# Kernel optimization log

Hardware: AMD Instinct MI355X
Metric: run time of the kernel (lower is better)

The kernel has to match this reference:

```python
import jax, jax.numpy as jnp
import numpy as np

D, H, E, K, N, PROJ = 512, 1024, 8, 2, 65536, 256
C = N * K // E  # expert capacity (capacity_factor=1.0 over the full token count)
LOG100 = float(np.log(100.0))


def _l2norm(v, axis=-1):
    return v / (jnp.linalg.norm(v, axis=axis, keepdims=True) + 1e-12)


def _moe(x, mask, Wp, bp, sim, temp, W1, b1, W2, b2):
    # tutel 'cosine_top' gate: cosine sim between projected tokens and expert embeddings,
    # scaled by clamped learned temperature.
    logits = _l2norm(x @ Wp + bp) @ _l2norm(sim, axis=0)
    logits = logits * jnp.exp(jnp.minimum(temp, LOG100))
    gates_all = jax.nn.softmax(logits, axis=-1)
    g, idx = jax.lax.top_k(gates_all, K)                      # [N,K]
    g = g / (jnp.sum(g, axis=-1, keepdims=True) + 1e-9)       # normalize top-k gates
    g = g * mask[:, None]                                     # zero out tokens not in this domain
    e = idx.reshape(-1)                                       # [N*K] expert id per slot
    gflat = g.reshape(-1)
    valid = jnp.repeat(mask, K)                               # [N*K]
    oh = jax.nn.one_hot(e, E, dtype=jnp.float32) * valid[:, None]
    pos = (jnp.cumsum(oh, axis=0) * oh).sum(-1).astype(jnp.int32) - 1  # slot within expert
    keep = ((pos >= 0) & (pos < C)).astype(x.dtype)           # drop overflow / masked tokens
    posc = jnp.clip(pos, 0, C - 1)
    tok = jnp.arange(N * K, dtype=jnp.int32) // K
    # dispatch -> [E,C,D]
    xd = jnp.zeros((E, C, D), x.dtype).at[e, posc].add(x[tok] * keep[:, None])
    # grouped expert FFN
    h = jax.nn.relu(jnp.einsum('ecd,edh->ech', xd, W1) + b1[:, None, :])
    y = jnp.einsum('ech,ehd->ecd', h, W2) + b2[:, None, :]
    # combine back to tokens
    out = jnp.zeros((N, D), x.dtype).at[tok].add(y[e, posc] * (gflat * keep)[:, None])
    return out


def _make_params(key):
    ks = jax.random.split(key, 4)
    Wp = jax.random.normal(ks[0], (D, PROJ), jnp.float32) * 0.02
    bp = jnp.zeros((PROJ,), jnp.float32)
    sim = jax.random.normal(ks[1], (PROJ, E), jnp.float32) * 0.02
    temp = jnp.asarray(np.log(10.0), jnp.float32)
    W1 = jax.random.normal(ks[2], (E, D, H), jnp.float32) * (1.0 / np.sqrt(D))
    b1 = jnp.zeros((E, H), jnp.float32)
    W2 = jax.random.normal(ks[3], (E, H, D), jnp.float32) * (1.0 / np.sqrt(H))
    b2 = jnp.zeros((E, D), jnp.float32)
    return Wp, bp, sim, temp, W1, b1, W2, b2


def setup_inputs():
    key = jax.random.key(0)
    kx, kl, k1, k2, k3, ksc = jax.random.split(key, 6)
    inp = {
        'x': jax.random.normal(kx, (N, D), jnp.float32),
        'domain_label': jax.random.randint(kl, (N,), 0, 2),
        'domain_scale': jax.random.normal(ksc, (1,), jnp.float32) * 0.1,
    }
    for name, k in (('sh', k1), ('day', k2), ('nt', k3)):
        Wp, bp, sim, temp, W1, b1, W2, b2 = _make_params(k)
        inp.update({name + '_Wp': Wp, name + '_bp': bp, name + '_sim': sim, name + '_temp': temp,
                    name + '_W1': W1, name + '_b1': b1, name + '_W2': W2, name + '_b2': b2})
    return inp


def reference(x, domain_label, domain_scale,
              sh_Wp, sh_bp, sh_sim, sh_temp, sh_W1, sh_b1, sh_W2, sh_b2,
              day_Wp, day_bp, day_sim, day_temp, day_W1, day_b1, day_W2, day_b2,
              nt_Wp, nt_bp, nt_sim, nt_temp, nt_W1, nt_b1, nt_W2, nt_b2):
    ones = jnp.ones((N,), jnp.float32)
    day = (domain_label == 0).astype(jnp.float32)
    night = (domain_label == 1).astype(jnp.float32)
    f_shared = _moe(x, ones, sh_Wp, sh_bp, sh_sim, sh_temp, sh_W1, sh_b1, sh_W2, sh_b2)
    f_domain = (_moe(x, day, day_Wp, day_bp, day_sim, day_temp, day_W1, day_b1, day_W2, day_b2)
                + _moe(x, night, nt_Wp, nt_bp, nt_sim, nt_temp, nt_W1, nt_b1, nt_W2, nt_b2))
    return f_shared + domain_scale * f_domain
```

## Files before the change

### kernel.cpp

```cpp
#include <hip/hip_runtime.h>

#define NTOK 65536
#define DDIM 512
#define HDIM 1024
#define NEXP 8
#define PROJ 256
#define CAP  16384
#define NSLOT (2*NTOK)
#define LOG100 4.605170185988091f

typedef __attribute__((ext_vector_type(8))) short bf16x8;
typedef __attribute__((ext_vector_type(4))) short short4v;
typedef __attribute__((ext_vector_type(4))) float f32x4;

__device__ inline float bf2f(unsigned short u){
    union { float f; unsigned int i; } c; c.i = ((unsigned int)u) << 16; return c.f;
}
__device__ inline unsigned short f2bf(float f){
    union { float f; unsigned int i; } c; c.f = f;
    unsigned int x = c.i;
    return (unsigned short)((x + 0x7fffu + ((x >> 16) & 1u)) >> 16);
}
__device__ inline void gload16(const void* g, void* lds){
    __builtin_amdgcn_global_load_lds(
        (const __attribute__((address_space(1))) unsigned int*)g,
        (__attribute__((address_space(3))) unsigned int*)lds, 16, 0, 0);
}

__global__ void init_k(const float4* __restrict__ x, ushort4* __restrict__ xb,
                       float4* __restrict__ out){
    long i = (long)blockIdx.x * 256 + threadIdx.x;
    float4 f = x[i];
    ushort4 u; u.x = f2bf(f.x); u.y = f2bf(f.y); u.z = f2bf(f.z); u.w = f2bf(f.w);
    xb[i] = u;
    out[i] = float4{0.f, 0.f, 0.f, 0.f};
}

__device__ inline void trans_body(const float* in, unsigned short* out, int R, int C){
    int rbase = blockIdx.y * 32, cbase = blockIdx.x * 32;
    if (rbase >= R || cbase >= C) return;
    __shared__ float tile[32][33];
    int tx = threadIdx.x, ty = threadIdx.y;
    #pragma unroll
    for (int i = 0; i < 4; i++)
        tile[ty + i*8][tx] = in[(long)(rbase + ty + i*8) * C + cbase + tx];
    __syncthreads();
    #pragma unroll
    for (int i = 0; i < 4; i++)
        out[(long)(cbase + ty + i*8) * R + rbase + tx] = f2bf(tile[tx][ty + i*8]);
}

__global__ __launch_bounds__(256)
void trans2_k(const float* __restrict__ W1, const float* __restrict__ W2,
              unsigned short* __restrict__ W1T, unsigned short* __restrict__ W2T)
{
    int z = blockIdx.z;
    if (z < 8) trans_body(W1 + (size_t)z*DDIM*HDIM, W1T + (size_t)z*DDIM*HDIM, DDIM, HDIM);
    else       trans_body(W2 + (size_t)(z-8)*DDIM*HDIM, W2T + (size_t)(z-8)*DDIM*HDIM, HDIM, DDIM);
}

struct W12P { const float* W1[3]; const float* W2[3]; };
__global__ __launch_bounds__(256)
void transW12all_k(W12P wp, unsigned short* __restrict__ W1T3, unsigned short* __restrict__ W2T3)
{
    int z = blockIdx.z, m = z >> 4, piece = z & 15;
    if (piece < 8)
        trans_body(wp.W1[m] + (size_t)piece*DDIM*HDIM,
                   W1T3 + ((size_t)m*8 + piece)*DDIM*HDIM, DDIM, HDIM);
    else
        trans_body(wp.W2[m] + (size_t)(piece-8)*DDIM*HDIM,
                   W2T3 + ((size_t)m*8 + piece-8)*DDIM*HDIM, HDIM, DDIM);
}

struct TpArgs { const float* Wp[3]; };
__global__ __launch_bounds__(256)
void transWp_k(TpArgs ta, unsigned short* __restrict__ WpT3)
{
    int m = blockIdx.z;
    trans_body(ta.Wp[m], WpT3 + (size_t)m*PROJ*DDIM, DDIM, PROJ);
}

struct SimArgs { const float* sim[3]; };
__global__ void simn3_k(SimArgs sa, float* __restrict__ simn3){
    __shared__ float red[256];
    const float* sim = sa.sim[blockIdx.x];
    float* simn = simn3 + (size_t)blockIdx.x * PROJ * NEXP;
    int j = threadIdx.x;
    for (int e = 0; e < NEXP; e++){
        float v = sim[j*NEXP + e];
        red[j] = v*v;
        __syncthreads();
        for (int s = 128; s > 0; s >>= 1){
            if (j < s) red[j] += red[j + s];
            __syncthreads();
        }
        float nrm = sqrtf(red[0]) + 1e-12f;
        __syncthreads();
        simn[j*NEXP + e] = v / nrm;
    }
}

struct WprodArgs { const float* Wp[3]; const float* bp[3]; };
__global__ __launch_bounds__(256)
void wprod_k(WprodArgs wa, const float* __restrict__ simn3,
             float* __restrict__ Wn3, float* __restrict__ bd3)
{
    int m = blockIdx.x;
    __shared__ float Sn[PROJ*NEXP];
    const float* Wp = wa.Wp[m];
    int t = threadIdx.x;
    for (int i = t; i < PROJ*NEXP; i += 256) Sn[i] = simn3[(size_t)m*PROJ*NEXP + i];
    __syncthreads();
    for (int r = t; r < DDIM; r += 256){
        float d[8];
        #pragma unroll
        for (int e = 0; e < 8; e++) d[e] = 0.f;
        for (int p = 0; p < PROJ; p++){
            float w = Wp[(size_t)r*PROJ + p];
            #pragma unroll
            for (int e = 0; e < 8; e++) d[e] = fmaf(w, Sn[p*8+e], d[e]);
        }
        #pragma unroll
        for (int e = 0; e < 8; e++) Wn3[((size_t)m*DDIM + r)*8 + e] = d[e];
    }
    if (t < 8){
        float s = 0.f;
        for (int p = 0; p < PROJ; p++) s = fmaf(wa.bp[m][p], Sn[p*8+t], s);
        bd3[m*8 + t] = s;
    }
}

struct PssArgs { const float* bp[3]; };
__global__ __launch_bounds__(256)
void pss_k(const unsigned short* __restrict__ WpT3, const unsigned short* __restrict__ xb,
           PssArgs pa, float* __restrict__ ssbuf)
{
    __shared__ __align__(16) short As[128*32];
    __shared__ __align__(16) short Bs[128*32];
    __shared__ float ssl[2][128];
    const int m = blockIdx.z;
    const int row0 = blockIdx.x * 128;
    const int n0 = blockIdx.y * 128;
    const unsigned short* AT = WpT3 + (size_t)m * PROJ * DDIM;
    const float* bp = pa.bp[m];

    const int t = threadIdx.x, w = t >> 6, l = t & 63;
    const int qrow = l >> 2, kc = (l & 3) * 8;
    long arowg[2], browg[2];
    #pragma unroll
    for (int q = 0; q < 2; q++){
        arowg[q] = (long)(row0 + w*32 + q*16 + qrow) * DDIM;
        browg[q] = (long)(n0   + w*32 + q*16 + qrow) * DDIM;
    }
    const int wm = (w >> 1) * 64, wn = (w & 1) * 64;
    const int fr = l & 15, fk = l >> 4;
    const int koff = fk * 8, fk4 = fk * 4;

    f32x4 acc[4][4];
    #pragma unroll
    for (int i = 0; i < 4; i++)
        #pragma unroll
        for (int j = 0; j < 4; j++) acc[i][j] = (f32x4){0.f, 0.f, 0.f, 0.f};

    for (int k0 = 0; k0 < DDIM; k0 += 32){
        __syncthreads();
        #pragma unroll
        for (int q = 0; q < 2; q++) gload16(AT + arowg[q] + k0 + kc, As + w*1024 + q*512);
        #pragma unroll
        for (int q = 0; q < 2; q++) gload16(xb + browg[q] + k0 + kc, Bs + w*1024 + q*512);
        __syncthreads();
        bf16x8 af[4], bfv[4];
        #pragma unroll
        for (int i = 0; i < 4; i++) af[i]  = *(const bf16x8*)&As[(wm + i*16 + fr)*32 + koff];
        #pragma unroll
        for (int j = 0; j < 4; j++) bfv[j] = *(const bf16x8*)&Bs[(wn + j*16 + fr)*32 + koff];
        #pragma unroll
        for (int i = 0; i < 4; i++)
            #pragma unroll
            for (int j = 0; j < 4; j++)
                acc[i][j] = __builtin_amdgcn_mfma_f32_16x16x32_bf16(af[i], bfv[j], acc[i][j], 0, 0, 0);
    }

    float part[4];
    #pragma unroll
    for (int j = 0; j < 4; j++){
        float s = 0.f;
        #pragma unroll
        for (int i = 0; i < 4; i++){
            int mc = row0 + wm + i*16 + fk4;
            float4 bb = *(const float4*)(bp + mc);
            float v0 = acc[i][j][0] + bb.x;
            float v1 = acc[i][j][1] + bb.y;
            float v2 = acc[i][j][2] + bb.z;
            float v3 = acc[i][j][3] + bb.w;
            s += v0*v0 + v1*v1 + v2*v2 + v3*v3;
        }
        s += __shfl_xor(s, 16, 64);
        s += __shfl_xor(s, 32, 64);
        part[j] = s;
    }
    if (fk == 0){
        #pragma unroll
        for (int j = 0; j < 4; j++) ssl[w >> 1][wn + j*16 + fr] = part[j];
    }
    __syncthreads();
    if (t < 128)
        ssbuf[((size_t)blockIdx.x*3 + m)*NTOK + n0 + t] = ssl[0][t] + ssl[1][t];
}

struct GfArgs { const float* tp[3]; };
__global__ __launch_bounds__(256)
void gatefin2_k(const float* __restrict__ x, const int* __restrict__ label,
                const float* __restrict__ Wn3, const float* __restrict__ bd3,
                const float* __restrict__ ssbuf, GfArgs gf,
                int* __restrict__ idx3, float* __restrict__ gw3)
{
    __shared__ __align__(16) float Wl[3*512*12];
    const int t = threadIdx.x;
    for (int i = t; i < 3072; i += 256){
        float4 v = ((const float4*)Wn3)[i];
        int row = i >> 1, half = i & 1;
        *(float4*)&Wl[row*12 + half*4] = v;
    }
    __syncthreads();

    const int r = t & 7, q = t >> 3;
    const int n0 = blockIdx.x * 128;
    const int nb = n0 + q*4;

    float dots[4][3][8];
    #pragma unroll
    for (int a = 0; a < 4; a++)
        #pragma unroll
        for (int m = 0; m < 3; m++)
            #pragma unroll
            for (int e = 0; e < 8; e++) dots[a][m][e] = 0.f;

    #pragma unroll 4
    for (int i = 0; i < 16; i++){
        float4 xv[4];
        #pragma unroll
        for (int a = 0; a < 4; a++)
            xv[a] = ((const float4*)(x + (size_t)(nb + a)*DDIM))[r + 8*i];
        #pragma unroll
        for (int j = 0; j < 4; j++){
            int k = (r + 8*i)*4 + j;
            #pragma unroll
            for (int m = 0; m < 3; m++){
                const float* wr = &Wl[(m*512 + k)*12];
                float4 w0 = *(const float4*)wr;
                float4 w1 = *(const float4*)(wr + 4);
                #pragma unroll
                for (int a = 0; a < 4; a++){
                    float av = (j==0) ? xv[a].x : (j==1) ? xv[a].y : (j==2) ? xv[a].z : xv[a].w;
                    dots[a][m][0] = fmaf(av, w0.x, dots[a][m][0]);
                    dots[a][m][1] = fmaf(av, w0.y, dots[a][m][1]);
                    dots[a][m][2] = fmaf(av, w0.z, dots[a][m][2]);
                    dots[a][m][3] = fmaf(av, w0.w, dots[a][m][3]);
                    dots[a][m][4] = fmaf(av, w1.x, dots[a][m][4]);
                    dots[a][m][5] = fmaf(av, w1.y, dots[a][m][5]);
                    dots[a][m][6] = fmaf(av, w1.z, dots[a][m][6]);
                    dots[a][m][7] = fmaf(av, w1.w, dots[a][m][7]);
                }
            }
        }
    }
    #pragma unroll
    for (int o = 1; o <= 4; o <<= 1)
        #pragma unroll
        for (int a = 0; a < 4; a++)
            #pragma unroll
            for (int m = 0; m < 3; m++)
                #pragma unroll
                for (int e = 0; e < 8; e++)
                    dots[a][m][e] += __shfl_xor(dots[a][m][e], o, 64);

    if (r == 0){
        #pragma unroll
        for (int a = 0; a < 4; a++){
            int n = nb + a;
            int lab = label[n];
            #pragma unroll
            for (int m = 0; m < 3; m++){
                float ss = ssbuf[(0*3+m)*(size_t)NTOK + n] + ssbuf[(1*3+m)*(size_t)NTOK + n];
                float scale = expf(fminf(gf.tp[m][0], LOG100));
                float inv = scale / (sqrtf(ss) + 1e-12f);
                float l8[8], mx = -1e30f;
                #pragma unroll
                for (int e = 0; e < 8; e++){
                    l8[e] = (dots[a][m][e] + bd3[m*8+e]) * inv;
                    mx = fmaxf(mx, l8[e]);
                }
                float g[8], s = 0.f;
                #pragma unroll
                for (int e = 0; e < 8; e++){ g[e] = expf(l8[e] - mx); s += g[e]; }
                #pragma unroll
                for (int e = 0; e < 8; e++) g[e] /= s;
                int e0 = 0; float b0 = g[0];
                #pragma unroll
                for (int e = 1; e < 8; e++) if (g[e] > b0){ b0 = g[e]; e0 = e; }
                int e1 = (e0 == 0) ? 1 : 0; float b1v = g[e1];
                #pragma unroll
                for (int e = 0; e < 8; e++) if (e != e0 && g[e] > b1v){ b1v = g[e]; e1 = e; }
                float maskv = (m == 0) ? 1.f : ((lab == m - 1) ? 1.f : 0.f);
                float s2 = b0 + b1v + 1e-9f;
                size_t base = (size_t)m * NSLOT + 2*(size_t)n;
                gw3[base]   = b0 / s2 * maskv;
                gw3[base+1] = b1v / s2 * maskv;
                idx3[base]   = e0;
                idx3[base+1] = e1;
            }
        }
    }
}

template<int BGATHER, int OMODE>
__device__ __forceinline__
void gemm_core_t(short* As, short* Bs,
                 const unsigned short* __restrict__ AT, const unsigned short* __restrict__ Bv,
                 const float* __restrict__ bias, void* __restrict__ Cout,
                 int Kd, int Mld, int row0, int col0, int limitN,
                 const int* __restrict__ rowidx, const int* __restrict__ otok,
                 const float* __restrict__ gs)
{
    const int t = threadIdx.x;
    const int w = t >> 6, l = t & 63;
    const int qrow = l >> 2;
    const int kc = (l & 3) * 8;

    long arowg[2], browg[2];
    #pragma unroll
    for (int q = 0; q < 2; q++){
        arowg[q] = (long)(row0 + w*32 + q*16 + qrow) * Kd;
        int s = col0 + w*32 + q*16 + qrow;
        int gi = s;
        if (BGATHER) gi = (s < limitN) ? rowidx[s] : 0;
        browg[q] = (long)gi * Kd;
    }

    const int wm = (w >> 1) * 64, wn = (w & 1) * 64;
    const int fr = l & 15, fk = l >> 4;
    const int koff = fk * 8, fk4 = fk * 4;

    f32x4 acc[4][4];
    #pragma unroll
    for (int i = 0; i < 4; i++)
        #pragma unroll
        for (int j = 0; j < 4; j++) acc[i][j] = (f32x4){0.f, 0.f, 0.f, 0.f};

    for (int k0 = 0; k0 < Kd; k0 += 32){
        __syncthreads();
        #pragma unroll
        for (int q = 0; q < 2; q++) gload16(AT + arowg[q] + k0 + kc, As + w*1024 + q*512);
        #pragma unroll
        for (int q = 0; q < 2; q++) gload16(Bv + browg[q] + k0 + kc, Bs + w*1024 + q*512);
        __syncthreads();
        bf16x8 af[4], bfv[4];
        #pragma unroll
        for (int i = 0; i < 4; i++) af[i]  = *(const bf16x8*)&As[(wm + i*16 + fr)*32 + koff];
        #pragma unroll
        for (int j = 0; j < 4; j++) bfv[j] = *(const bf16x8*)&Bs[(wn + j*16 + fr)*32 + koff];
        #pragma unroll
        for (int i = 0; i < 4; i++)
            #pragma unroll
            for (int j = 0; j < 4; j++)
                acc[i][j] = __builtin_amdgcn_mfma_f32_16x16x32_bf16(af[i], bfv[j], acc[i][j], 0, 0, 0);
    }

    #pragma unroll
    for (int i = 0; i < 4; i++){
        const int mc = row0 + wm + i*16 + fk4;
        float4 bb = *(const float4*)(bias + mc);
        #pragma unroll
        for (int j = 0; j < 4; j++){
            int s = col0 + wn + j*16 + fr;
            if (s < limitN){
                if (OMODE == 1){
                    ushort4 u;
                    u.x = f2bf(fmaxf(acc[i][j][0] + bb.x, 0.f));
                    u.y = f2bf(fmaxf(acc[i][j][1] + bb.y, 0.f));
                    u.z = f2bf(fmaxf(acc[i][j][2] + bb.z, 0.f));
                    u.w = f2bf(fmaxf(acc[i][j][3] + bb.w, 0.f));
                    *(ushort4*)((unsigned short*)Cout + (long)s * Mld + mc) = u;
                } else {
                    int tk = otok[s];
                    float g = gs[s];
                    float* op = (float*)Cout + (long)tk * Mld + mc;
                    float4 c = *(const float4*)op;
                    c.x += g * (acc[i][j][0] + bb.x);
                    c.y += g * (acc[i][j][1] + bb.y);
                    c.z += g * (acc[i][j][2] + bb.z);
                    c.w += g * (acc[i][j][3] + bb.w);
                    *(float4*)op = c;
                }
            }
        }
    }
}

template<int BGATHER, int OMODE>
__device__ __forceinline__
void gemm_core_t64(short* As, short* Bs,
                   const unsigned short* __restrict__ AT, const unsigned short* __restrict__ Bv,
                   const float* __restrict__ bias, void* __restrict__ Cout,
                   int Kd, int Mld, int row0, int col0, int limitN,
                   const int* __restrict__ rowidx, const int* __restrict__ otok,
                   const float* __restrict__ gs)
{
    const int t = threadIdx.x;
    const int w = t >> 6, l = t & 63;
    const int qrow = l >> 2;
    const int seg = (l & 3) * 8;

    long arowg[2], browg[2];
    #pragma unroll
    for (int q = 0; q < 2; q++){
        arowg[q] = (long)(row0 + w*32 + q*16 + qrow) * Kd;
        int s = col0 + w*32 + q*16 + qrow;
        int gi = s;
        if (BGATHER) gi = (s < limitN) ? rowidx[s] : 0;
        browg[q] = (long)gi * Kd;
    }

    const int wm = (w >> 1) * 64, wn = (w & 1) * 64;
    const int fr = l & 15, fk = l >> 4;
    const int koff = fk * 8, fk4 = fk * 4;

    f32x4 acc[4][4];
    #pragma unroll
    for (int i = 0; i < 4; i++)
        #pragma unroll
        for (int j = 0; j < 4; j++) acc[i][j] = (f32x4){0.f, 0.f, 0.f, 0.f};

    for (int k0 = 0; k0 < Kd; k0 += 64){
        __syncthreads();
        #pragma unroll
        for (int ks = 0; ks < 2; ks++)
            #pragma unroll
            for (int q = 0; q < 2; q++)
                gload16(AT + arowg[q] + k0 + ks*32 + seg, As + ks*4096 + w*1024 + q*512);
        #pragma unroll
        for (int ks = 0; ks < 2; ks++)
            #pragma unroll
            for (int q = 0; q < 2; q++)
                gload16(Bv + browg[q] + k0 + ks*32 + seg, Bs + ks*4096 + w*1024 + q*512);
        __syncthreads();
        #pragma unroll
        for (int ks = 0; ks < 2; ks++){
            bf16x8 af[4], bfv[4];
            #pragma unroll
            for (int i = 0; i < 4; i++) af[i]  = *(const bf16x8*)&As[ks*4096 + (wm + i*16 + fr)*32 + koff];
            #pragma unroll
            for (int j = 0; j < 4; j++) bfv[j] = *(const bf16x8*)&Bs[ks*4096 + (wn + j*16 + fr)*32 + koff];
            #pragma unroll
            for (int i = 0; i < 4; i++)
                #pragma unroll
                for (int j = 0; j < 4; j++)
                    acc[i][j] = __builtin_amdgcn_mfma_f32_16x16x32_bf16(af[i], bfv[j], acc[i][j], 0, 0, 0);
        }
    }

    #pragma unroll
    for (int i = 0; i < 4; i++){
        const int mc = row0 + wm + i*16 + fk4;
        float4 bb = *(const float4*)(bias + mc);
        #pragma unroll
        for (int j = 0; j < 4; j++){
            int s = col0 + wn + j*16 + fr;
            if (s < limitN){
                if (OMODE == 1){
                    ushort4 u;
                    u.x = f2bf(fmaxf(acc[i][j][0] + bb.x, 0.f));
                    u.y = f2bf(fmaxf(acc[i][j][1] + bb.y, 0.f));
                    u.z = f2bf(fmaxf(acc[i][j][2] + bb.z, 0.f));
                    u.w = f2bf(fmaxf(acc[i][j][3] + bb.w, 0.f));
                    *(ushort4*)((unsigned short*)Cout + (long)s * Mld + mc) = u;
                } else {
                    int tk = otok[s];
                    float g = gs[s];
                    float* op = (float*)Cout + (long)tk * Mld + mc;
                    float4 c = *(const float4*)op;
                    c.x += g * (acc[i][j][0] + bb.x);
                    c.y += g * (acc[i][j][1] + bb.y);
                    c.z += g * (acc[i][j][2] + bb.z);
                    c.w += g * (acc[i][j][3] + bb.w);
                    *(float4*)op = c;
                }
            }
        }
    }
}

__device__ __forceinline__
void gemm_core_y64(short* lds,
                   const unsigned short* __restrict__ AT, const unsigned short* __restrict__ Bv,
                   const float* __restrict__ bias, float* __restrict__ out,
                   int row0, int col0, int limitN,
                   const int* __restrict__ otok, const float* __restrict__ gs)
{
    short* As = lds;
    short* Bs = lds + 4096;
    const int t = threadIdx.x, w = t >> 6, l = t & 63;
    const int seg = (l & 3) * 8;

    const long arow = (long)(row0 + w*16 + (l >> 2)) * HDIM;
    long brow[2];
    #pragma unroll
    for (int hh = 0; hh < 2; hh++)
        brow[hh] = (long)(col0 + w*32 + hh*16 + (l >> 2)) * HDIM;

    const int wm = (w >> 1) * 32, wn = (w & 1) * 64;
    const int fr = l & 15, fk = l >> 4;
    const int koff = fk * 8, fk4 = fk * 4;

    f32x4 acc[2][4];
    #pragma unroll
    for (int i = 0; i < 2; i++)
        #pragma unroll
        for (int j = 0; j < 4; j++) acc[i][j] = (f32x4){0.f, 0.f, 0.f, 0.f};

    for (int k0 = 0; k0 < HDIM; k0 += 64){
        __syncthreads();
        #pragma unroll
        for (int ks = 0; ks < 2; ks++)
            gload16(AT + arow + k0 + ks*32 + seg, As + ks*2048 + w*512);
        #pragma unroll
        for (int ks = 0; ks < 2; ks++)
            #pragma unroll
            for (int hh = 0; hh < 2; hh++)
                gload16(Bv + brow[hh] + k0 + ks*32 + seg, Bs + ks*4096 + w*1024 + hh*512);
        __syncthreads();
        #pragma unroll
        for (int ks = 0; ks < 2; ks++){
            bf16x8 af[2], bfv[4];
            #pragma unroll
            for (int i = 0; i < 2; i++)
                af[i] = *(const bf16x8*)&As[ks*2048 + (wm + i*16 + fr)*32 + koff];
            #pragma unroll
            for (int j = 0; j < 4; j++)
                bfv[j] = *(const bf16x8*)&Bs[ks*4096 + (wn + j*16 + fr)*32 + koff];
            #pragma unroll
            for (int i = 0; i < 2; i++)
                #pragma unroll
                for (int j = 0; j < 4; j++)
                    acc[i][j] = __builtin_amdgcn_mfma_f32_16x16x32_bf16(af[i], bfv[j], acc[i][j], 0, 0, 0);
        }
    }

    #pragma unroll
    for (int i = 0; i < 2; i++){
        const int mc = row0 + wm + i*16 + fk4;
        float4 bb = *(const float4*)(bias + mc);
        #pragma unroll
        for (int j = 0; j < 4; j++){
            int s = col0 + wn + j*16 + fr;
            if (s < limitN){
                int tk = otok[s];
                float g = gs[s];
                float* op = out + (long)tk * DDIM + mc;
                float4 c = *(const float4*)op;
                c.x += g * (acc[i][j][0] + bb.x);
                c.y += g * (acc[i][j][1] + bb.y);
                c.z += g * (acc[i][j][2] + bb.z);
                c.w += g * (acc[i][j][3] + bb.w);
                *(float4*)op = c;
            }
        }
    }
}

template<int BGATHER, int OMODE>
__global__ __launch_bounds__(256)
void mgemm3_k(const unsigned short* __restrict__ AT, const unsigned short* __restrict__ Bv,
              const float* __restrict__ bias, void* __restrict__ Cout,
              int Kd, int Mld,
              const int* __restrict__ rowidx, const int* __restrict__ otok,
              const float* __restrict__ gs, const int* __restrict__ cntp, int cnti)
{
    __shared__ __align__(16) short As[128*32];
    __shared__ __align__(16) short Bs[128*32];
    int limit = cntp[cnti]; if (limit > CAP) limit = CAP;
    int row0 = blockIdx.x * 128, col0 = blockIdx.y * 128;
    if (col0 >= limit) return;
    gemm_core_t<BGATHER, OMODE>(As, Bs, AT, Bv, bias, Cout, Kd, Mld,
                                row0, col0, limit, rowidx, otok, gs);
}

struct FfnP { const float* b1[3]; const float* b2[3]; };
__global__ __launch_bounds__(256)
void ffnA_k(const unsigned short* __restrict__ xb,
            const unsigned short* __restrict__ W1T3, const unsigned short* __restrict__ W2T3,
            FfnP fp, unsigned short* __restrict__ h0, unsigned short* __restrict__ h1,
            float* __restrict__ out,
            const int* __restrict__ tok3, const float* __restrict__ gslot3,
            const int* __restrict__ cntk3, int ge)
{
    __shared__ __align__(16) short lds[16384];
    const int bx = blockIdx.x, by = blockIdx.y;
    const int col0 = bx * 128;
    if (by < 8){
        if (ge >= 24) return;
        int m = ge >> 3, e = ge & 7;
        int limit = cntk3[m*16 + e]; if (limit > CAP) limit = CAP;
        if (col0 >= limit) return;
        unsigned short* hd = (ge & 1) ? h1 : h0;
        gemm_core_t64<1, 1>(lds, lds + 8192,
                            W1T3 + ((size_t)(m*8+e))*HDIM*DDIM, xb, fp.b1[m] + (size_t)e*HDIM,
                            hd, DDIM, HDIM, by*128, col0, limit,
                            tok3 + ((size_t)m*NEXP + e)*CAP, nullptr, nullptr);
    } else {
        int gy = ge - 1; if (gy < 0) return;
        int m = gy >> 3, e = gy & 7;
        int limit = cntk3[m*16 + e]; if (limit > CAP) limit = CAP;
        if (col0 >= limit) return;
        const unsigned short* hs = (gy & 1) ? h1 : h0;
        gemm_core_y64(lds, W2T3 + ((size_t)(m*8+e))*DDIM*HDIM, hs, fp.b2[m] + (size_t)e*DDIM,
                      out, (by-8)*64, col0, limit,
                      tok3 + ((size_t)m*NEXP + e)*CAP, gslot3 + ((size_t)m*NEXP + e)*CAP);
    }
}

__global__ __launch_bounds__(256)
void ffnB_k(const unsigned short* __restrict__ xb,
            const unsigned short* __restrict__ W1T, const float* __restrict__ b1,
            const unsigned short* __restrict__ W2T, const float* __restrict__ b2,
            unsigned short* __restrict__ h0, unsigned short* __restrict__ h1,
            float* __restrict__ out,
            const int* __restrict__ tok, const float* __restrict__ gslot,
            const int* __restrict__ cntk, int eh)
{
    __shared__ __align__(16) short lds[12288];
    const int bx = blockIdx.x, by = blockIdx.y;
    const int col0 = bx * 128;
    if (by < 8){
        if (eh > 7) return;
        int limit = cntk[eh]; if (limit > CAP) limit = CAP;
        if (col0 >= limit) return;
        unsigned short* hd = (eh & 1) ? h1 : h0;
        gemm_core_t<1, 1>(lds, lds + 4096,
                          W1T + (size_t)eh*HDIM*DDIM, xb, b1 + (size_t)eh*HDIM,
                          hd, DDIM, HDIM, by*128, col0, limit,
                          tok + (size_t)eh*CAP, nullptr, nullptr);
    } else {
        int ey = eh - 1; if (ey < 0) return;
        int limit = cntk[ey]; if (limit > CAP) limit = CAP;
        if (col0 >= limit) return;
        const unsigned short* hs = (ey & 1) ? h1 : h0;
        gemm_core_y64(lds, W2T + (size_t)ey*DDIM*HDIM, hs, b2 + (size_t)ey*DDIM,
                      out, (by-8)*64, col0, limit,
                      tok + (size_t)ey*CAP, gslot + (size_t)ey*CAP);
    }
}

__global__ __launch_bounds__(1024)
void rank_count3_k(const int* __restrict__ idx3, const int* __restrict__ label,
                   int* __restrict__ bcnt3)
{
    __shared__ int c[NEXP];
    const int m = blockIdx.y;
    const int* idx = idx3 + (size_t)m * NSLOT;
    int t = threadIdx.x;
    if (t < NEXP) c[t] = 0;
    __syncthreads();
    int s = blockIdx.x * 1024 + t;
    int n = s >> 1;
    int e = idx[s];
    bool valid = (m == 0) || (label[n] == m - 1);
    if (valid) atomicAdd(&c[e], 1);
    __syncthreads();
    if (t < NEXP) bcnt3[((size_t)m*128 + blockIdx.x)*NEXP + t] = c[t];
}

__global__ void rank_scan3_k(const int* __restrict__ bcnt3, int* __restrict__ boff3,
                             int* __restrict__ cntk3)
{
    int m = blockIdx.x, e = threadIdx.x;
    if (e < NEXP){
        int run = 0;
        for (int b = 0; b < NSLOT/1024; b++){
            boff3[((size_t)m*128 + b)*NEXP + e] = run;
            run += bcnt3[((size_t)m*128 + b)*NEXP + e];
        }
        cntk3[m*16 + e] = run < CAP ? run : CAP;
    }
}

__global__ __launch_bounds__(1024)
void rank_assign3_k(const int* __restrict__ idx3, const int* __restrict__ label,
                    const int* __restrict__ boff3, const float* __restrict__ gw3,
                    const float* __restrict__ dscale,
                    int* __restrict__ tok3, float* __restrict__ gs3)
{
    __shared__ int wcnt[16][NEXP];
    __shared__ int woff[16][NEXP];
    const int m = blockIdx.y;
    const int* idx = idx3 + (size_t)m * NSLOT;
    const float* gw = gw3 + (size_t)m * NSLOT;
    int t = threadIdx.x;
    int s = blockIdx.x * 1024 + t;
    int n = s >> 1;
    int e = idx[s];
    bool valid = (m == 0) || (label[n] == m - 1);
    int w = t >> 6, lane = t & 63;
    unsigned long long lt = (lane == 0) ? 0ull : ((1ull << lane) - 1ull);
    int myrank = 0;
    #pragma unroll
    for (int ei = 0; ei < NEXP; ei++){
        unsigned long long bal = __ballot(valid && (e == ei));
        if (ei == e) myrank = __popcll(bal & lt);
        if (lane == 0) wcnt[w][ei] = __popcll(bal);
    }
    __syncthreads();
    if (t < NEXP){
        int run = boff3[((size_t)m*128 + blockIdx.x)*NEXP + t];
        for (int w2 = 0; w2 < 16; w2++){
            woff[w2][t] = run;
            run += wcnt[w2][t];
        }
    }
    __syncthreads();
    int pos = woff[w][e] + myrank;
    bool keep = valid && (pos < CAP);
    if (keep){
        float scale = (m > 0) ? dscale[0] : 1.f;
        tok3[((size_t)m*NEXP + e)*CAP + pos] = n;
        gs3[((size_t)m*NEXP + e)*CAP + pos] = gw[s] * scale;
    }
}

extern "C" void kernel_launch(void* const* d_in, const int* in_sizes, int n_in,
                              void* d_out, int out_size, void* d_ws, size_t ws_size,
                              hipStream_t stream)
{
    (void)in_sizes; (void)n_in; (void)out_size;
    const float* x      = (const float*)d_in[0];
    const int*   label  = (const int*)  d_in[1];
    const float* dscale = (const float*)d_in[2];
    float* out = (float*)d_out;

    const size_t XB  = (size_t)NTOK * DDIM * 2;
    const size_t HS  = (size_t)CAP * HDIM * 2;
    const size_t WPT = (size_t)3 * PROJ * DDIM * 2;
    const size_t SS  = (size_t)2 * 3 * NTOK * 4;
    const size_t WN  = (size_t)3 * DDIM * 8 * 4;
    const size_t SMALL = WPT + SS + WN + 256 +
                         (size_t)3*PROJ*NEXP*4 +
                         (size_t)3*NSLOT*4*2 +
                         (size_t)3*NEXP*CAP*4*2 +
                         (size_t)3*128*NEXP*4*2 + 256;
    const size_t W12A = (size_t)2 * 3 * NEXP * DDIM * HDIM * 2;
    const size_t W12B = (size_t)2 * NEXP * DDIM * HDIM * 2;
    const size_t common = XB + HS + SMALL;

    int tier;
    if      (ws_size >= common + HS + W12A) tier = 0;
    else if (ws_size >= common + HS + W12B) tier = 1;
    else if (ws_size >= common + W12B)      tier = 2;
    else return;

    char* p = (char*)d_ws;
    unsigned short* xb   = (unsigned short*)p; p += XB;
    unsigned short* h0   = (unsigned short*)p; p += HS;
    unsigned short* WpT3 = (unsigned short*)p; p += WPT;
    float* ssbuf = (float*)p;  p += SS;
    float* Wn3   = (float*)p;  p += WN;
    float* bd3   = (float*)p;  p += 256;
    float* simn3 = (float*)p;  p += (size_t)3*PROJ*NEXP*4;
    int*   idx3  = (int*)p;    p += (size_t)3*NSLOT*4;
    float* gw3   = (float*)p;  p += (size_t)3*NSLOT*4;
    int*   tok3  = (int*)p;    p += (size_t)3*NEXP*CAP*4;
    float* gslot3= (float*)p;  p += (size_t)3*NEXP*CAP*4;
    int*   bcnt3 = (int*)p;    p += (size_t)3*128*NEXP*4;
    int*   boff3 = (int*)p;    p += (size_t)3*128*NEXP*4;
    int*   cntk3 = (int*)p;    p += 256;
    unsigned short* h1 = nullptr;
    if (tier <= 1){ h1 = (unsigned short*)p; p += HS; }
    unsigned short* Wbuf = (unsigned short*)p;

    SimArgs sa; TpArgs ta; WprodArgs wa; PssArgs pa; GfArgs gf; W12P wp; FfnP fp;
    for (int m = 0; m < 3; m++){
        ta.Wp[m] = (const float*)d_in[3 + 8*m + 0];
        wa.Wp[m] = ta.Wp[m];
        wa.bp[m] = (const float*)d_in[3 + 8*m + 1];
        pa.bp[m] = wa.bp[m];
        sa.sim[m] = (const float*)d_in[3 + 8*m + 2];
        gf.tp[m] = (const float*)d_in[3 + 8*m + 3];
        wp.W1[m] = (const float*)d_in[3 + 8*m + 4];
        fp.b1[m] = (const float*)d_in[3 + 8*m + 5];
        wp.W2[m] = (const float*)d_in[3 + 8*m + 6];
        fp.b2[m] = (const float*)d_in[3 + 8*m + 7];
    }

    init_k<<<dim3(NTOK*DDIM/4/256), dim3(256), 0, stream>>>(
        (const float4*)x, (ushort4*)xb, (float4*)out);
    simn3_k<<<dim3(3), dim3(256), 0, stream>>>(sa, simn3);
    transWp_k<<<dim3(PROJ/32, DDIM/32, 3), dim3(32,8), 0, stream>>>(ta, WpT3);
    wprod_k<<<dim3(3), dim3(256), 0, stream>>>(wa, simn3, Wn3, bd3);
    pss_k<<<dim3(2, NTOK/128, 3), dim3(256), 0, stream>>>(WpT3, xb, pa, ssbuf);
    gatefin2_k<<<dim3(NTOK/128), dim3(256), 0, stream>>>(
        x, label, Wn3, bd3, ssbuf, gf, idx3, gw3);

    rank_count3_k<<<dim3(NSLOT/1024, 3), dim3(1024), 0, stream>>>(idx3, label, bcnt3);
    rank_scan3_k<<<dim3(3), dim3(64), 0, stream>>>(bcnt3, boff3, cntk3);
    rank_assign3_k<<<dim3(NSLOT/1024, 3), dim3(1024), 0, stream>>>(
        idx3, label, boff3, gw3, dscale, tok3, gslot3);

    if (tier == 0){
        unsigned short* W1T3 = Wbuf;
        unsigned short* W2T3 = Wbuf + (size_t)3*NEXP*DDIM*HDIM;
        transW12all_k<<<dim3(32, 32, 48), dim3(32,8), 0, stream>>>(wp, W1T3, W2T3);
        for (int ge = 0; ge <= 24; ge++)
            ffnA_k<<<dim3(128, 16), 256, 0, stream>>>(
                xb, W1T3, W2T3, fp, h0, h1, out, tok3, gslot3, cntk3, ge);
    } else {
        unsigned short* W1T = Wbuf;
        unsigned short* W2T = Wbuf + (size_t)NEXP*DDIM*HDIM;
        for (int m = 0; m < 3; m++){
            trans2_k<<<dim3(32, 32, 16), dim3(32,8), 0, stream>>>(wp.W1[m], wp.W2[m], W1T, W2T);
            const int* tokm = tok3 + (size_t)m*NEXP*CAP;
            const float* gsm = gslot3 + (size_t)m*NEXP*CAP;
            const int* cntm = cntk3 + m*16;
            if (tier == 1){
                for (int eh = 0; eh <= 8; eh++)
                    ffnB_k<<<dim3(128, 16), 256, 0, stream>>>(
                        xb, W1T, fp.b1[m], W2T, fp.b2[m], h0, h1, out, tokm, gsm, cntm, eh);
            } else {
                for (int e = 0; e < NEXP; e++){
                    mgemm3_k<1, 1><<<dim3(HDIM/128, CAP/128), 256, 0, stream>>>(
                        W1T + (size_t)e*HDIM*DDIM, xb, fp.b1[m] + (size_t)e*HDIM, h0,
                        DDIM, HDIM, tokm + (size_t)e*CAP, nullptr, nullptr, cntm, e);
                    mgemm3_k<0, 3><<<dim3(DDIM/128, CAP/128), 256, 0, stream>>>(
                        W2T + (size_t)e*DDIM*HDIM, h0, fp.b2[m] + (size_t)e*DDIM, out,
                        HDIM, DDIM, nullptr, tokm + (size_t)e*CAP, gsm + (size_t)e*CAP, cntm, e);
                }
            }
        }
    }
}
```

Baseline: 1.850 ms.

## Restructure gate dot-product kernel and use 128-wide tiles for second FFN GEMM

The gate-finish kernel now gives each thread one token and a quarter of the feature dimension, reading the small normalized weight matrix straight from global/cache instead of staging it in LDS. Partial dot products are reduced through a small LDS buffer rather than cross-lane shuffles, with 64 tokens per block. Separately, the second expert GEMM in ffnA switches from the 64-row output core to the generic 128-row templated core (OMODE 3, scatter-add), which cuts the y-dimension of the grid from 16 to 12. These changes aim to cut gate overhead and improve GEMM tile efficiency, at the cost of uncoalesced per-token x loads and more register pressure in the larger tiles.

```diff
diff --git a/kernel.cpp b/kernel.cpp
--- a/kernel.cpp
+++ b/kernel.cpp
@@ -210,106 +210,94 @@
 
 struct GfArgs { const float* tp[3]; };
 __global__ __launch_bounds__(256)
-void gatefin2_k(const float* __restrict__ x, const int* __restrict__ label,
+void gatefin3_k(const float* __restrict__ x, const int* __restrict__ label,
                 const float* __restrict__ Wn3, const float* __restrict__ bd3,
                 const float* __restrict__ ssbuf, GfArgs gf,
                 int* __restrict__ idx3, float* __restrict__ gw3)
 {
-    __shared__ __align__(16) float Wl[3*512*12];
+    __shared__ float pd[3][64][26];
     const int t = threadIdx.x;
-    for (int i = t; i < 3072; i += 256){
-        float4 v = ((const float4*)Wn3)[i];
-        int row = i >> 1, half = i & 1;
-        *(float4*)&Wl[row*12 + half*4] = v;
-    }
-    __syncthreads();
-
-    const int r = t & 7, q = t >> 3;
-    const int n0 = blockIdx.x * 128;
-    const int nb = n0 + q*4;
-
-    float dots[4][3][8];
-    #pragma unroll
-    for (int a = 0; a < 4; a++)
-        #pragma unroll
-        for (int m = 0; m < 3; m++)
-            #pragma unroll
-            for (int e = 0; e < 8; e++) dots[a][m][e] = 0.f;
-
-    #pragma unroll 4
-    for (int i = 0; i < 16; i++){
+    const int tok = t & 63;
+    const int qu = __builtin_amdgcn_readfirstlane(t >> 6);
+    const int n = blockIdx.x * 64 + tok;
+
+    float dots[3][8];
+    #pragma unroll
+    for (int m = 0; m < 3; m++)
+        #pragma unroll
+        for (int e = 0; e < 8; e++) dots[m][e] = 0.f;
+
+    const float4* xp = (const float4*)(x + (size_t)n * DDIM + qu * 128);
+    for (int c = 0; c < 8; c++){
         float4 xv[4];
         #pragma unroll
-        for (int a = 0; a < 4; a++)
-            xv[a] = ((const float4*)(x + (size_t)(nb + a)*DDIM))[r + 8*i];
-        #pragma unroll
-        for (int j = 0; j < 4; j++){
-            int k = (r + 8*i)*4 + j;
+        for (int u = 0; u < 4; u++) xv[u] = xp[c*4 + u];
+        #pragma unroll
+        for (int kk = 0; kk < 16; kk++){
+            float a = (kk & 2) ? ((kk & 1) ? xv[kk>>2].w : xv[kk>>2].z)
+                               : ((kk & 1) ? xv[kk>>2].y : xv[kk>>2].x);
+            int k = qu*128 + c*16 + kk;
             #pragma unroll
             for (int m = 0; m < 3; m++){
-                const float* wr = &Wl[(m*512 + k)*12];
+                const float* wr = Wn3 + ((size_t)m*DDIM + k)*8;
                 float4 w0 = *(const float4*)wr;
                 float4 w1 = *(const float4*)(wr + 4);
-                #pragma unroll
-                for (int a = 0; a < 4; a++){
-                    float av = (j==0) ? xv[a].x : (j==1) ? xv[a].y : (j==2) ? xv[a].z : xv[a].w;
-                    dots[a][m][0] = fmaf(av, w0.x, dots[a][m][0]);
-                    dots[a][m][1] = fmaf(av, w0.y, dots[a][m][1]);
-                    dots[a][m][2] = fmaf(av, w0.z, dots[a][m][2]);
-                    dots[a][m][3] = fmaf(av, w0.w, dots[a][m][3]);
-                    dots[a][m][4] = fmaf(av, w1.x, dots[a][m][4]);
-                    dots[a][m][5] = fmaf(av, w1.y, dots[a][m][5]);
-                    dots[a][m][6] = fmaf(av, w1.z, dots[a][m][6]);
-                    dots[a][m][7] = fmaf(av, w1.w, dots[a][m][7]);
-                }
+                dots[m][0] = fmaf(a, w0.x, dots[m][0]);
+                dots[m][1] = fmaf(a, w0.y, dots[m][1]);
+                dots[m][2] = fmaf(a, w0.z, dots[m][2]);
+                dots[m][3] = fmaf(a, w0.w, dots[m][3]);
+                dots[m][4] = fmaf(a, w1.x, dots[m][4]);
+                dots[m][5] = fmaf(a, w1.y, dots[m][5]);
+                dots[m][6] = fmaf(a, w1.z, dots[m][6]);
+                dots[m][7] = fmaf(a, w1.w, dots[m][7]);
             }
         }
     }
-    #pragma unroll
-    for (int o = 1; o <= 4; o <<= 1)
-        #pragma unroll
-        for (int a = 0; a < 4; a++)
+    if (qu != 0){
+        #pragma unroll
+        for (int m = 0; m < 3; m++)
+            #pragma unroll
+            for (int e = 0; e < 8; e++) pd[qu-1][tok][m*8+e] = dots[m][e];
+    }
+    __syncthreads();
+    if (qu == 0){
+        #pragma unroll
+        for (int qq = 0; qq < 3; qq++)
             #pragma unroll
             for (int m = 0; m < 3; m++)
                 #pragma unroll
-                for (int e = 0; e < 8; e++)
-                    dots[a][m][e] += __shfl_xor(dots[a][m][e], o, 64);
-
-    if (r == 0){
-        #pragma unroll
-        for (int a = 0; a < 4; a++){
-            int n = nb + a;
-            int lab = label[n];
-            #pragma unroll
-            for (int m = 0; m < 3; m++){
-                float ss = ssbuf[(0*3+m)*(size_t)NTOK + n] + ssbuf[(1*3+m)*(size_t)NTOK + n];
-                float scale = expf(fminf(gf.tp[m][0], LOG100));
-                float inv = scale / (sqrtf(ss) + 1e-12f);
-                float l8[8], mx = -1e30f;
-                #pragma unroll
-                for (int e = 0; e < 8; e++){
-                    l8[e] = (dots[a][m][e] + bd3[m*8+e]) * inv;
-                    mx = fmaxf(mx, l8[e]);
-                }
-                float g[8], s = 0.f;
-                #pragma unroll
-                for (int e = 0; e < 8; e++){ g[e] = expf(l8[e] - mx); s += g[e]; }
-                #pragma unroll
-                for (int e = 0; e < 8; e++) g[e] /= s;
-                int e0 = 0; float b0 = g[0];
-                #pragma unroll
-                for (int e = 1; e < 8; e++) if (g[e] > b0){ b0 = g[e]; e0 = e; }
-                int e1 = (e0 == 0) ? 1 : 0; float b1v = g[e1];
-                #pragma unroll
-                for (int e = 0; e < 8; e++) if (e != e0 && g[e] > b1v){ b1v = g[e]; e1 = e; }
-                float maskv = (m == 0) ? 1.f : ((lab == m - 1) ? 1.f : 0.f);
-                float s2 = b0 + b1v + 1e-9f;
-                size_t base = (size_t)m * NSLOT + 2*(size_t)n;
-                gw3[base]   = b0 / s2 * maskv;
-                gw3[base+1] = b1v / s2 * maskv;
-                idx3[base]   = e0;
-                idx3[base+1] = e1;
+                for (int e = 0; e < 8; e++) dots[m][e] += pd[qq][tok][m*8+e];
+
+        int lab = label[n];
+        #pragma unroll
+        for (int m = 0; m < 3; m++){
+            float ss = ssbuf[(0*3+m)*(size_t)NTOK + n] + ssbuf[(1*3+m)*(size_t)NTOK + n];
+            float scale = expf(fminf(gf.tp[m][0], LOG100));
+            float inv = scale / (sqrtf(ss) + 1e-12f);
+            float l8[8], mx = -1e30f;
+            #pragma unroll
+            for (int e = 0; e < 8; e++){
+                l8[e] = (dots[m][e] + bd3[m*8+e]) * inv;
+                mx = fmaxf(mx, l8[e]);
             }
+            float g[8], s = 0.f;
+            #pragma unroll
+            for (int e = 0; e < 8; e++){ g[e] = expf(l8[e] - mx); s += g[e]; }
+            #pragma unroll
+            for (int e = 0; e < 8; e++) g[e] /= s;
+            int e0 = 0; float b0 = g[0];
+            #pragma unroll
+            for (int e = 1; e < 8; e++) if (g[e] > b0){ b0 = g[e]; e0 = e; }
+            int e1 = (e0 == 0) ? 1 : 0; float b1v = g[e1];
+            #pragma unroll
+            for (int e = 0; e < 8; e++) if (e != e0 && g[e] > b1v){ b1v = g[e]; e1 = e; }
+            float maskv = (m == 0) ? 1.f : ((lab == m - 1) ? 1.f : 0.f);
+            float s2 = b0 + b1v + 1e-9f;
+            size_t base = (size_t)m * NSLOT + 2*(size_t)n;
+            gw3[base]   = b0 / s2 * maskv;
+            gw3[base+1] = b1v / s2 * maskv;
+            idx3[base]   = e0;
+            idx3[base+1] = e1;
         }
     }
 }
@@ -614,9 +602,11 @@
         int limit = cntk3[m*16 + e]; if (limit > CAP) limit = CAP;
         if (col0 >= limit) return;
         const unsigned short* hs = (gy & 1) ? h1 : h0;
-        gemm_core_y64(lds, W2T3 + ((size_t)(m*8+e))*DDIM*HDIM, hs, fp.b2[m] + (size_t)e*DDIM,
-                      out, (by-8)*64, col0, limit,
-                      tok3 + ((size_t)m*NEXP + e)*CAP, gslot3 + ((size_t)m*NEXP + e)*CAP);
+        gemm_core_t64<0, 3>(lds, lds + 8192,
+                            W2T3 + ((size_t)(m*8+e))*DDIM*HDIM, hs, fp.b2[m] + (size_t)e*DDIM,
+                            out, HDIM, DDIM, (by-8)*128, col0, limit,
+                            nullptr, tok3 + ((size_t)m*NEXP + e)*CAP,
+                            gslot3 + ((size_t)m*NEXP + e)*CAP);
     }
 }
 
@@ -797,7 +787,7 @@
     transWp_k<<<dim3(PROJ/32, DDIM/32, 3), dim3(32,8), 0, stream>>>(ta, WpT3);
     wprod_k<<<dim3(3), dim3(256), 0, stream>>>(wa, simn3, Wn3, bd3);
     pss_k<<<dim3(2, NTOK/128, 3), dim3(256), 0, stream>>>(WpT3, xb, pa, ssbuf);
-    gatefin2_k<<<dim3(NTOK/128), dim3(256), 0, stream>>>(
+    gatefin3_k<<<dim3(NTOK/64), dim3(256), 0, stream>>>(
         x, label, Wn3, bd3, ssbuf, gf, idx3, gw3);
 
     rank_count3_k<<<dim3(NSLOT/1024, 3), dim3(1024), 0, stream>>>(idx3, label, bcnt3);
@@ -810,7 +800,7 @@
         unsigned short* W2T3 = Wbuf + (size_t)3*NEXP*DDIM*HDIM;
         transW12all_k<<<dim3(32, 32, 48), dim3(32,8), 0, stream>>>(wp, W1T3, W2T3);
         for (int ge = 0; ge <= 24; ge++)
-            ffnA_k<<<dim3(128, 16), 256, 0, stream>>>(
+            ffnA_k<<<dim3(128, 12), 256, 0, stream>>>(
                 xb, W1T3, W2T3, fp, h0, h1, out, tok3, gslot3, cntk3, ge);
     } else {
         unsigned short* W1T = Wbuf;
```

Result: no change. 1.863 ms (+0.7%).
